# Kernel tuning notes

Measured on AMD Instinct MI355X. Metric: run time of the kernel, lower is better.

The kernel has to match this reference:

```python
import jax, jax.numpy as jnp
import numpy as np

K = 3
STRIDE = 1
PAD = 1


def conv2d(x, w, b):
    # standard NCHW conv, stride 1, pad 1
    out = jax.lax.conv_general_dilated(
        x, w, (STRIDE, STRIDE), [(PAD, PAD), (PAD, PAD)],
        dimension_numbers=("NCHW", "OIHW", "NCHW"))
    return out + b[None, :, None, None]


def deform_conv2d(x, offset, mask, weight):
    # torchvision.ops.deform_conv2d semantics (offset_groups=1):
    # offset: [B, 2*K*K, Ho, Wo] laid out as (k, (y, x)) per kernel tap k (row-major)
    # mask:   [B, K*K, Ho, Wo]
    B, C, H, W = x.shape
    KK = K * K
    Ho, Wo = offset.shape[2:]
    off = offset.reshape(B, KK, 2, Ho, Wo)

    # base sampling positions: p = out*stride - pad + kernel_tap + offset
    tap_y = jnp.repeat(jnp.arange(K, dtype=x.dtype), K)  # [KK]
    tap_x = jnp.tile(jnp.arange(K, dtype=x.dtype), K)    # [KK]
    grid_y = jnp.arange(Ho, dtype=x.dtype) * STRIDE - PAD
    grid_x = jnp.arange(Wo, dtype=x.dtype) * STRIDE - PAD
    py = grid_y[None, None, :, None] + tap_y[None, :, None, None] + off[:, :, 0]  # [B,KK,Ho,Wo]
    px = grid_x[None, None, None, :] + tap_x[None, :, None, None] + off[:, :, 1]

    y0 = jnp.floor(py)
    x0 = jnp.floor(px)
    wy1 = py - y0  # fractional parts
    wx1 = px - x0

    xf = x.reshape(B, C, H * W)

    def gather(yi, xi):
        # zero-padding semantics: out-of-bounds corners contribute 0
        valid = (yi >= 0) & (yi <= H - 1) & (xi >= 0) & (xi <= W - 1)
        idx = (jnp.clip(yi, 0, H - 1) * W + jnp.clip(xi, 0, W - 1)).astype(jnp.int32)
        v = jnp.take_along_axis(xf, idx.reshape(B, 1, KK * Ho * Wo), axis=2)
        v = v.reshape(B, C, KK, Ho, Wo)
        return v * valid[:, None].astype(x.dtype)

    e = lambda a: a[:, None]  # [B,KK,Ho,Wo] -> [B,1,KK,Ho,Wo]
    sampled = (gather(y0, x0) * e((1 - wy1) * (1 - wx1))
               + gather(y0, x0 + 1) * e((1 - wy1) * wx1)
               + gather(y0 + 1, x0) * e(wy1 * (1 - wx1))
               + gather(y0 + 1, x0 + 1) * e(wy1 * wx1))
    sampled = sampled * mask[:, None]  # modulated, [B,C,KK,Ho,Wo]

    Cout = weight.shape[0]
    out = jnp.einsum("bckhw,ock->bohw", sampled, weight.reshape(Cout, C, KK))
    return out


def setup_inputs() -> dict:
    key = jax.random.key(0)
    ks = jax.random.split(key, 5)
    B, Cin, Cout, H, W = 4, 128, 256, 64, 64
    x = jax.random.normal(ks[0], (B, Cin, H, W), jnp.float32)
    # offset/modulator convs are zero-init in the module; use small random weights
    # so the deformable sampling path is actually exercised
    offset_w = jax.random.normal(ks[1], (2 * K * K, Cin, K, K), jnp.float32) * 0.02
    offset_b = jax.random.normal(ks[2], (2 * K * K,), jnp.float32) * 0.1
    mod_w = jax.random.normal(ks[3], (K * K, Cin, K, K), jnp.float32) * 0.02
    mod_b = jnp.zeros((K * K,), jnp.float32)
    weight = jax.random.normal(ks[4], (Cout, Cin, K, K), jnp.float32) * (1.0 / np.sqrt(Cin * K * K))
    return {"x": x, "offset_w": offset_w, "offset_b": offset_b,
            "mod_w": mod_w, "mod_b": mod_b, "weight": weight}


def reference(x, offset_w, offset_b, mod_w, mod_b, weight):
    H, W = x.shape[2], x.shape[3]
    max_offset = max(H, W) / 4.0
    offset = jnp.clip(conv2d(x, offset_w, offset_b), -max_offset, max_offset)
    mask = 2.0 * jax.nn.sigmoid(conv2d(x, mod_w, mod_b))
    return deform_conv2d(x, offset, mask, weight)
```

## Files before the change

### kernel.cpp

```cpp
#include <hip/hip_runtime.h>
#include <math.h>

#define CIN   128
#define COUT  256
#define HH    64
#define WW    64
#define BB    4
#define KK    9
#define CK    (CIN*KK)

typedef unsigned short u16;
typedef unsigned int   u32;
using f32x4  = __attribute__((ext_vector_type(4))) float;
using s16x8  = __attribute__((ext_vector_type(8))) short;

__device__ __forceinline__ u16 f2bf(float f) {
    union { float f; u32 u; } v; v.f = f;
    u32 u = v.u;
    u += 0x7FFFu + ((u >> 16) & 1u);
    return (u16)(u >> 16);
}
__device__ __forceinline__ float bflo(u32 u) {
    union { u32 u; float f; } v; v.u = u << 16;
    return v.f;
}
__device__ __forceinline__ float bfhi(u32 u) {
    union { u32 u; float f; } v; v.u = u & 0xFFFF0000u;
    return v.f;
}

__global__ __launch_bounds__(256)
void prep_all(const float* __restrict__ x, const float* __restrict__ w,
              const float* __restrict__ ow, const float* __restrict__ mw,
              u16* __restrict__ xt, u16* __restrict__ wfrag,
              u16* __restrict__ wofsf) {
    __shared__ u16 T[64][130];
    int blk = blockIdx.x;
    int tid = threadIdx.x;

    if (blk < 256) {
        int b = blk >> 6, y = blk & 63;
        int lane = tid & 63, cw = tid >> 6;
        for (int c = cw; c < 128; c += 4)
            T[lane][c] = f2bf(x[((b * 128 + c) * 64 + y) * 64 + lane]);
        __syncthreads();
        int c = tid & 127;
        for (int p = tid >> 7; p < 64; p += 2)
            xt[((b * 64 + y) * 64 + p) * 128 + c] = T[p][c];
    } else if (blk < 256 + 1152) {
        int i = (blk - 256) * 256 + tid;
        int j     = i & 7;
        int lane  = (i >> 3) & 63;
        int ks    = (i >> 9) & 1;
        int ct    = (i >> 10) & 3;
        int q     = (i >> 12) & 3;
        int chunk = i >> 14;
        int co  = q * 64 + ct * 16 + (lane & 15);
        int k   = chunk * 64 + ks * 32 + (lane >> 4) * 8 + j;
        int tap = k >> 7, c = k & 127;
        wfrag[i] = f2bf(w[co * CK + c * 9 + tap]);
    } else {
        int i = (blk - 1408) * 256 + tid;
        if (i < 32 * CK) {
            int j     = i & 7;
            int lane  = (i >> 3) & 63;
            int ks    = (i >> 9) & 1;
            int t     = (i >> 10) & 1;
            int chunk = i >> 11;
            int co  = t * 16 + (lane & 15);
            int k   = chunk * 64 + ks * 32 + (lane >> 4) * 8 + j;
            int tap = k >> 7, c = k & 127;
            float v = 0.f;
            if (co < 18)      v = ow[co * CK + c * 9 + tap];
            else if (co < 27) v = mw[(co - 18) * CK + c * 9 + tap];
            wofsf[i] = f2bf(v);
        }
    }
}

__global__ __launch_bounds__(512, 4)
void dcn_fused(const u16* __restrict__ xt, const u16* __restrict__ wofsf,
               const float* __restrict__ ob, const float* __restrict__ mb,
               const u16* __restrict__ wfrag, float* __restrict__ out) {
    int blkid = blockIdx.x;
    int xcd = blkid & 7, idx = blkid >> 3;
    int b   = xcd >> 1;
    int ho  = ((xcd & 1) << 5) + (idx >> 1);
    int wo0 = (idx & 1) << 5;
    int tid = threadIdx.x;

    __shared__ u16   Sm[2][32][72];
    __shared__ float s_om[27][32];
    __shared__ int   s_idx[32][KK][4];
    __shared__ float s_wgt[32][KK][4];

    int wv   = tid >> 6, lane = tid & 63;
    int quad = lane >> 4, l16 = lane & 15;

    int cp    = tid & 31;
    int pslot = tid >> 5;

    const u16* xtb = xt + (size_t)b * 4096 * 128;

    int pa_ph = wv & 1;
    f32x4 aco[2];
    aco[0] = (f32x4)(0.f); aco[1] = (f32x4)(0.f);

    u32 ra[2];
    auto pa_gather = [&](int chunk) {
        int tap = chunk >> 1, cb = chunk & 1;
        int kx = tap % 3;
        int y  = ho - 1 + tap / 3;
        bool yok = (y >= 0) && (y < HH);
#pragma unroll
        for (int s = 0; s < 2; ++s) {
            int px  = 2 * pslot + s;
            int col = wo0 + px + kx - 1;
            bool ok = yok && ((unsigned)col < WW);
            ra[s] = ok ? *(const u32*)(xtb + (size_t)(y * 64 + col) * 128 + cb * 64 + 2 * cp)
                       : 0u;
        }
    };

    pa_gather(0);
    int buf = 0;
    for (int chunk = 0; chunk < 18; ++chunk) {
        *(u32*)(&Sm[buf][2 * pslot][2 * cp])     = ra[0];
        *(u32*)(&Sm[buf][2 * pslot + 1][2 * cp]) = ra[1];
        __syncthreads();
        if (chunk < 17) pa_gather(chunk + 1);

        const u16* wc = wofsf + chunk * 2048 + lane * 8;
#pragma unroll
        for (int ks = 0; ks < 2; ++ks) {
            s16x8 bfrag = *(const s16x8*)(&Sm[buf][pa_ph * 16 + l16][ks * 32 + quad * 8]);
#pragma unroll
            for (int t = 0; t < 2; ++t) {
                s16x8 afrag = *(const s16x8*)(wc + (t * 2 + ks) * 512);
                aco[t] = __builtin_amdgcn_mfma_f32_16x16x32_bf16(afrag, bfrag, aco[t], 0, 0, 0);
            }
        }
        buf ^= 1;
    }
    if (wv < 2) {
#pragma unroll
        for (int t = 0; t < 2; ++t) {
#pragma unroll
            for (int r = 0; r < 4; ++r) {
                int co = t * 16 + quad * 4 + r;
                if (co < 27) {
                    float v = aco[t][r];
                    if (co < 18) {
                        v += ob[co];
                        v = fminf(fmaxf(v, -16.f), 16.f);
                    } else {
                        v += mb[co - 18];
                        v = 2.f / (1.f + expf(-v));
                    }
                    s_om[co][pa_ph * 16 + l16] = v;
                }
            }
        }
    }
    __syncthreads();

    if (tid < 32 * KK) {
        int p = tid / KK, k = tid - (tid / KK) * KK;
        int wo = wo0 + p;
        float offy = s_om[2 * k][p];
        float offx = s_om[2 * k + 1][p];
        float mval = s_om[18 + k][p];

        float py = (float)(ho - 1 + k / 3) + offy;
        float px = (float)(wo - 1 + k % 3) + offx;
        float y0f = floorf(py), x0f = floorf(px);
        float wy1 = py - y0f,  wx1 = px - x0f;
        float wy0 = 1.f - wy1, wx0 = 1.f - wx1;
        int iy0 = (int)y0f, ix0 = (int)x0f;
        int iy1 = iy0 + 1,  ix1 = ix0 + 1;
        bool vy0 = (iy0 >= 0) && (iy0 < HH);
        bool vy1 = (iy1 >= 0) && (iy1 < HH);
        bool vx0 = (ix0 >= 0) && (ix0 < WW);
        bool vx1 = (ix1 >= 0) && (ix1 < WW);
        int cy0 = min(max(iy0, 0), HH - 1), cy1 = min(max(iy1, 0), HH - 1);
        int cx0 = min(max(ix0, 0), WW - 1), cx1 = min(max(ix1, 0), WW - 1);
        s_idx[p][k][0] = (cy0 * WW + cx0) * 128;
        s_idx[p][k][1] = (cy0 * WW + cx1) * 128;
        s_idx[p][k][2] = (cy1 * WW + cx0) * 128;
        s_idx[p][k][3] = (cy1 * WW + cx1) * 128;
        s_wgt[p][k][0] = (vy0 && vx0) ? mval * wy0 * wx0 : 0.f;
        s_wgt[p][k][1] = (vy0 && vx1) ? mval * wy0 * wx1 : 0.f;
        s_wgt[p][k][2] = (vy1 && vx0) ? mval * wy1 * wx0 : 0.f;
        s_wgt[p][k][3] = (vy1 && vx1) ? mval * wy1 * wx1 : 0.f;
    }
    __syncthreads();

    const u16* wq = wfrag + lane * 8;

    f32x4 acc[2][2];
#pragma unroll
    for (int t = 0; t < 2; ++t) { acc[t][0] = (f32x4)(0.f); acc[t][1] = (f32x4)(0.f); }

    float vlo[2], vhi[2];
    auto gather = [&](int chunk) {
        int tap = chunk >> 1, cb = chunk & 1;
        int coff = cb * 64 + 2 * cp;
#pragma unroll
        for (int s = 0; s < 2; ++s) {
            int p = 2 * pslot + s;
            int   i0 = s_idx[p][tap][0], i1 = s_idx[p][tap][1];
            int   i2 = s_idx[p][tap][2], i3 = s_idx[p][tap][3];
            float g0 = s_wgt[p][tap][0], g1 = s_wgt[p][tap][1];
            float g2 = s_wgt[p][tap][2], g3 = s_wgt[p][tap][3];
            u32 u0 = *(const u32*)(xtb + i0 + coff);
            u32 u1 = *(const u32*)(xtb + i1 + coff);
            u32 u2 = *(const u32*)(xtb + i2 + coff);
            u32 u3 = *(const u32*)(xtb + i3 + coff);
            vlo[s] = g0 * bflo(u0) + g1 * bflo(u1) + g2 * bflo(u2) + g3 * bflo(u3);
            vhi[s] = g0 * bfhi(u0) + g1 * bfhi(u1) + g2 * bfhi(u2) + g3 * bfhi(u3);
        }
    };

    gather(0);
    buf = 0;
    for (int chunk = 0; chunk < 18; ++chunk) {
        *(u32*)(&Sm[buf][2 * pslot][2 * cp]) =
            (u32)f2bf(vlo[0]) | ((u32)f2bf(vhi[0]) << 16);
        *(u32*)(&Sm[buf][2 * pslot + 1][2 * cp]) =
            (u32)f2bf(vlo[1]) | ((u32)f2bf(vhi[1]) << 16);
        __syncthreads();

        const u16* wc = wq + chunk * 16384;
        s16x8 af[4];
#pragma unroll
        for (int t = 0; t < 2; ++t)
#pragma unroll
            for (int ks = 0; ks < 2; ++ks)
                af[t * 2 + ks] = *(const s16x8*)(wc + ((wv * 2 + t) * 2 + ks) * 512);

        if (chunk < 17) gather(chunk + 1);

#pragma unroll
        for (int ks = 0; ks < 2; ++ks) {
            s16x8 bf0 = *(const s16x8*)(&Sm[buf][l16][ks * 32 + quad * 8]);
            s16x8 bf1 = *(const s16x8*)(&Sm[buf][16 + l16][ks * 32 + quad * 8]);
#pragma unroll
            for (int t = 0; t < 2; ++t) {
                acc[t][0] = __builtin_amdgcn_mfma_f32_16x16x32_bf16(af[t * 2 + ks], bf0, acc[t][0], 0, 0, 0);
                acc[t][1] = __builtin_amdgcn_mfma_f32_16x16x32_bf16(af[t * 2 + ks], bf1, acc[t][1], 0, 0, 0);
            }
        }
        buf ^= 1;
    }

#pragma unroll
    for (int t = 0; t < 2; ++t) {
        int cobase = (wv * 2 + t) * 16 + quad * 4;
#pragma unroll
        for (int ph = 0; ph < 2; ++ph) {
#pragma unroll
            for (int r = 0; r < 4; ++r) {
                int co = cobase + r;
                out[((b * COUT + co) * HH + ho) * WW + wo0 + ph * 16 + l16] = acc[t][ph][r];
            }
        }
    }
}

extern "C" void kernel_launch(void* const* d_in, const int* in_sizes, int n_in,
                              void* d_out, int out_size, void* d_ws, size_t ws_size,
                              hipStream_t stream) {
    const float* x  = (const float*)d_in[0];
    const float* ow = (const float*)d_in[1];
    const float* ob = (const float*)d_in[2];
    const float* mw = (const float*)d_in[3];
    const float* mb = (const float*)d_in[4];
    const float* wt = (const float*)d_in[5];

    char* ws = (char*)d_ws;
    u16* wfrag = (u16*)ws;  ws += (size_t)COUT * CK * 2;
    u16* wofsf = (u16*)ws;  ws += (size_t)32 * CK * 2;
    u16* xt    = (u16*)ws;
    float* out = (float*)d_out;

    prep_all<<<1552, 256, 0, stream>>>(x, wt, ow, mw, xt, wfrag, wofsf);

    dcn_fused<<<BB * HH * 2, 512, 0, stream>>>(xt, wofsf, ob, mb, wfrag, out);
}
```

Measured before the change: 111.8 us.

## Gather full 128-channel tap rows with 16-byte loads, halving loop iterations

Both the offset/mask conv and the deformable main loop now process one full tap (all 128 channels) per iteration instead of half-tap chunks. Each thread loads 8 channels per corner with a 16-byte vector load instead of 4-byte loads, and the shared tile is widened to 136 columns. This halves the number of barriers and iterations and makes global gathers wider. The offset-conv MFMAs are also restricted to the two waves that use them. In exchange, register pressure rises: 8 weight fragments and four 16-byte corner vectors are held per thread, which may hurt occupancy at the 512x4 launch bound.

```diff
diff --git a/kernel.cpp b/kernel.cpp
--- a/kernel.cpp
+++ b/kernel.cpp
@@ -20,13 +20,11 @@
     u += 0x7FFFu + ((u >> 16) & 1u);
     return (u16)(u >> 16);
 }
-__device__ __forceinline__ float bflo(u32 u) {
-    union { u32 u; float f; } v; v.u = u << 16;
-    return v.f;
-}
-__device__ __forceinline__ float bfhi(u32 u) {
-    union { u32 u; float f; } v; v.u = u & 0xFFFF0000u;
-    return v.f;
+__device__ __forceinline__ float bfel(s16x8 v, int j) {
+    union { u32 u; float f; } c; c.u = ((u32)(u16)v[j]) << 16; return c.f;
+}
+__device__ __forceinline__ u32 pk2(float a, float b) {
+    return (u32)f2bf(a) | ((u32)f2bf(b) << 16);
 }
 
 __global__ __launch_bounds__(256)
@@ -89,55 +87,54 @@
     int wo0 = (idx & 1) << 5;
     int tid = threadIdx.x;
 
-    __shared__ u16   Sm[2][32][72];
+    __shared__ __align__(16) u16 Sm[2][32][136];
     __shared__ float s_om[27][32];
     __shared__ int   s_idx[32][KK][4];
     __shared__ float s_wgt[32][KK][4];
 
     int wv   = tid >> 6, lane = tid & 63;
     int quad = lane >> 4, l16 = lane & 15;
-
-    int cp    = tid & 31;
-    int pslot = tid >> 5;
+    int gpx  = wv * 4 + (lane >> 4);
+    int oct  = lane & 15;
 
     const u16* xtb = xt + (size_t)b * 4096 * 128;
+    const s16x8 vzero = {0,0,0,0,0,0,0,0};
 
     int pa_ph = wv & 1;
     f32x4 aco[2];
     aco[0] = (f32x4)(0.f); aco[1] = (f32x4)(0.f);
 
-    u32 ra[2];
-    auto pa_gather = [&](int chunk) {
-        int tap = chunk >> 1, cb = chunk & 1;
+    s16x8 sa;
+    auto pa_gather = [&](int tap) {
         int kx = tap % 3;
         int y  = ho - 1 + tap / 3;
-        bool yok = (y >= 0) && (y < HH);
-#pragma unroll
-        for (int s = 0; s < 2; ++s) {
-            int px  = 2 * pslot + s;
-            int col = wo0 + px + kx - 1;
-            bool ok = yok && ((unsigned)col < WW);
-            ra[s] = ok ? *(const u32*)(xtb + (size_t)(y * 64 + col) * 128 + cb * 64 + 2 * cp)
-                       : 0u;
-        }
+        bool yok = (unsigned)y < HH;
+        int col = wo0 + gpx + kx - 1;
+        bool ok = yok && ((unsigned)col < WW);
+        int yc = yok ? y : 0;
+        int cc = ((unsigned)col < WW) ? col : 0;
+        sa = *(const s16x8*)(xtb + (size_t)(yc * 64 + cc) * 128 + oct * 8);
+        if (!ok) sa = vzero;
     };
 
     pa_gather(0);
     int buf = 0;
-    for (int chunk = 0; chunk < 18; ++chunk) {
-        *(u32*)(&Sm[buf][2 * pslot][2 * cp])     = ra[0];
-        *(u32*)(&Sm[buf][2 * pslot + 1][2 * cp]) = ra[1];
+    for (int tap = 0; tap < 9; ++tap) {
+        *(s16x8*)(&Sm[buf][gpx][oct * 8]) = sa;
         __syncthreads();
-        if (chunk < 17) pa_gather(chunk + 1);
-
-        const u16* wc = wofsf + chunk * 2048 + lane * 8;
-#pragma unroll
-        for (int ks = 0; ks < 2; ++ks) {
-            s16x8 bfrag = *(const s16x8*)(&Sm[buf][pa_ph * 16 + l16][ks * 32 + quad * 8]);
-#pragma unroll
-            for (int t = 0; t < 2; ++t) {
-                s16x8 afrag = *(const s16x8*)(wc + (t * 2 + ks) * 512);
-                aco[t] = __builtin_amdgcn_mfma_f32_16x16x32_bf16(afrag, bfrag, aco[t], 0, 0, 0);
+        if (tap < 8) pa_gather(tap + 1);
+
+        if (wv < 2) {
+            const u16* wc = wofsf + lane * 8;
+#pragma unroll
+            for (int ks4 = 0; ks4 < 4; ++ks4) {
+                int chunkA = tap * 2 + (ks4 >> 1);
+                s16x8 bfrag = *(const s16x8*)(&Sm[buf][pa_ph * 16 + l16][ks4 * 32 + quad * 8]);
+#pragma unroll
+                for (int t = 0; t < 2; ++t) {
+                    s16x8 afrag = *(const s16x8*)(wc + ((chunkA * 2 + t) * 2 + (ks4 & 1)) * 512);
+                    aco[t] = __builtin_amdgcn_mfma_f32_16x16x32_bf16(afrag, bfrag, aco[t], 0, 0, 0);
+                }
             }
         }
         buf ^= 1;
@@ -201,53 +198,54 @@
 #pragma unroll
     for (int t = 0; t < 2; ++t) { acc[t][0] = (f32x4)(0.f); acc[t][1] = (f32x4)(0.f); }
 
-    float vlo[2], vhi[2];
-    auto gather = [&](int chunk) {
-        int tap = chunk >> 1, cb = chunk & 1;
-        int coff = cb * 64 + 2 * cp;
-#pragma unroll
-        for (int s = 0; s < 2; ++s) {
-            int p = 2 * pslot + s;
-            int   i0 = s_idx[p][tap][0], i1 = s_idx[p][tap][1];
-            int   i2 = s_idx[p][tap][2], i3 = s_idx[p][tap][3];
-            float g0 = s_wgt[p][tap][0], g1 = s_wgt[p][tap][1];
-            float g2 = s_wgt[p][tap][2], g3 = s_wgt[p][tap][3];
-            u32 u0 = *(const u32*)(xtb + i0 + coff);
-            u32 u1 = *(const u32*)(xtb + i1 + coff);
-            u32 u2 = *(const u32*)(xtb + i2 + coff);
-            u32 u3 = *(const u32*)(xtb + i3 + coff);
-            vlo[s] = g0 * bflo(u0) + g1 * bflo(u1) + g2 * bflo(u2) + g3 * bflo(u3);
-            vhi[s] = g0 * bfhi(u0) + g1 * bfhi(u1) + g2 * bfhi(u2) + g3 * bfhi(u3);
-        }
+    s16x8 cr0, cr1, cr2, cr3;
+    float gg0, gg1, gg2, gg3;
+    auto gatherB = [&](int tap) {
+        int i0 = s_idx[gpx][tap][0], i1 = s_idx[gpx][tap][1];
+        int i2 = s_idx[gpx][tap][2], i3 = s_idx[gpx][tap][3];
+        gg0 = s_wgt[gpx][tap][0]; gg1 = s_wgt[gpx][tap][1];
+        gg2 = s_wgt[gpx][tap][2]; gg3 = s_wgt[gpx][tap][3];
+        int co8 = oct * 8;
+        cr0 = *(const s16x8*)(xtb + i0 + co8);
+        cr1 = *(const s16x8*)(xtb + i1 + co8);
+        cr2 = *(const s16x8*)(xtb + i2 + co8);
+        cr3 = *(const s16x8*)(xtb + i3 + co8);
     };
 
-    gather(0);
+    gatherB(0);
     buf = 0;
-    for (int chunk = 0; chunk < 18; ++chunk) {
-        *(u32*)(&Sm[buf][2 * pslot][2 * cp]) =
-            (u32)f2bf(vlo[0]) | ((u32)f2bf(vhi[0]) << 16);
-        *(u32*)(&Sm[buf][2 * pslot + 1][2 * cp]) =
-            (u32)f2bf(vlo[1]) | ((u32)f2bf(vhi[1]) << 16);
+    for (int tap = 0; tap < 9; ++tap) {
+        float o[8];
+#pragma unroll
+        for (int j = 0; j < 8; ++j)
+            o[j] = gg0 * bfel(cr0, j) + gg1 * bfel(cr1, j)
+                 + gg2 * bfel(cr2, j) + gg3 * bfel(cr3, j);
+        uint4 pkv;
+        pkv.x = pk2(o[0], o[1]); pkv.y = pk2(o[2], o[3]);
+        pkv.z = pk2(o[4], o[5]); pkv.w = pk2(o[6], o[7]);
+        *(uint4*)(&Sm[buf][gpx][oct * 8]) = pkv;
         __syncthreads();
 
-        const u16* wc = wq + chunk * 16384;
-        s16x8 af[4];
+        s16x8 af[8];
 #pragma unroll
         for (int t = 0; t < 2; ++t)
 #pragma unroll
-            for (int ks = 0; ks < 2; ++ks)
-                af[t * 2 + ks] = *(const s16x8*)(wc + ((wv * 2 + t) * 2 + ks) * 512);
-
-        if (chunk < 17) gather(chunk + 1);
-
-#pragma unroll
-        for (int ks = 0; ks < 2; ++ks) {
-            s16x8 bf0 = *(const s16x8*)(&Sm[buf][l16][ks * 32 + quad * 8]);
-            s16x8 bf1 = *(const s16x8*)(&Sm[buf][16 + l16][ks * 32 + quad * 8]);
+            for (int ks4 = 0; ks4 < 4; ++ks4) {
+                int chunkB = tap * 2 + (ks4 >> 1);
+                af[t * 4 + ks4] = *(const s16x8*)(
+                    wq + ((chunkB * 16 + (wv * 2 + t)) * 2 + (ks4 & 1)) * 512);
+            }
+
+        if (tap < 8) gatherB(tap + 1);
+
+#pragma unroll
+        for (int ks4 = 0; ks4 < 4; ++ks4) {
+            s16x8 bf0 = *(const s16x8*)(&Sm[buf][l16][ks4 * 32 + quad * 8]);
+            s16x8 bf1 = *(const s16x8*)(&Sm[buf][16 + l16][ks4 * 32 + quad * 8]);
 #pragma unroll
             for (int t = 0; t < 2; ++t) {
-                acc[t][0] = __builtin_amdgcn_mfma_f32_16x16x32_bf16(af[t * 2 + ks], bf0, acc[t][0], 0, 0, 0);
-                acc[t][1] = __builtin_amdgcn_mfma_f32_16x16x32_bf16(af[t * 2 + ks], bf1, acc[t][1], 0, 0, 0);
+                acc[t][0] = __builtin_amdgcn_mfma_f32_16x16x32_bf16(af[t * 4 + ks4], bf0, acc[t][0], 0, 0, 0);
+                acc[t][1] = __builtin_amdgcn_mfma_f32_16x16x32_bf16(af[t * 4 + ks4], bf1, acc[t][1], 0, 0, 0);
             }
         }
         buf ^= 1;
```

After: 103.8 us. 1.08x faster.
